# Optimization experiments

Hardware: AMD Instinct MI355X
Metric: run time of the kernel (lower is better)

The kernel has to match this reference:

```python
import jax, jax.numpy as jnp
import numpy as np

B, IN, N, E = 2048, 1024, 64, 128
NEG_SLOPE = 0.01  # torch LeakyReLU default

def setup_inputs() -> dict:
    key = jax.random.key(0)
    k = jax.random.split(key, 5)
    scale_in = 1.0 / np.sqrt(IN)
    scale_ctx = 1.0 / np.sqrt(2 * E)
    return {
        "x": jax.random.normal(k[0], (B, IN), dtype=jnp.float32),
        # stacked per-concept Linear(in_features, 2*emb_size)
        "W_ctx": jax.random.uniform(k[1], (N, IN, 2 * E), jnp.float32, -scale_in, scale_in),
        "b_ctx": jax.random.uniform(k[2], (N, 2 * E), jnp.float32, -scale_in, scale_in),
        # shared Linear(2*emb_size, 1)
        "w_prob": jax.random.uniform(k[3], (2 * E,), jnp.float32, -scale_ctx, scale_ctx),
        "b_prob": jax.random.uniform(k[4], (), jnp.float32, -scale_ctx, scale_ctx),
    }

def reference(x, W_ctx, b_ctx, w_prob, b_prob):
    # context: [B, N, 2E] = LeakyReLU(x @ W_i + b_i) for all concepts i at once
    ctx = jnp.einsum("bi,nio->bno", x, W_ctx) + b_ctx
    ctx = jnp.where(ctx >= 0, ctx, NEG_SLOPE * ctx)
    # shared gate: [B, N]
    c_pred = jax.nn.sigmoid(jnp.einsum("bno,o->bn", ctx, w_prob) + b_prob)
    # gated blend of positive/negative halves -> [B, N, E]
    p = c_pred[..., None]
    c_emb = ctx[..., :E] * p + ctx[..., E:] * (1.0 - p)
    return c_emb, c_pred
```

## Files before the change

### kernel.cpp

```cpp
#include <hip/hip_runtime.h>
#include <hip/hip_bf16.h>

typedef __attribute__((ext_vector_type(4))) short short4v;
typedef __attribute__((ext_vector_type(8))) short short8v;
typedef __attribute__((ext_vector_type(4))) float floatx4;

#define B_ROWS 2048
#define K_DIM  1024
#define N_CON  64
#define TWO_E  256
#define E_DIM  128
#define BM     128
#define BK     64
#define LDSA_BYTES (BM * BK * 2)
#define LDSB_BYTES (TWO_E * BK * 2)
#define SMEM_BYTES (LDSA_BYTES + LDSB_BYTES)
#define EMB_ELEMS 16777216ULL
#define WT_BYTES  33554432ULL
#define XB_BYTES  4194304ULL

static __device__ inline unsigned short bf16bits(float f) {
    __hip_bfloat16 h = __float2bfloat16(f);
    unsigned short u;
    __builtin_memcpy(&u, &h, 2);
    return u;
}

static __device__ inline void dma16(const void* g, void* l) {
    __builtin_amdgcn_global_load_lds(
        (const __attribute__((address_space(1))) unsigned int*)g,
        (__attribute__((address_space(3))) unsigned int*)l,
        16, 0, 0);
}

__global__ void __launch_bounds__(256) prep(const float* __restrict__ W,
                                            const float* __restrict__ x,
                                            unsigned short* __restrict__ Wt,
                                            unsigned short* __restrict__ xb) {
    __shared__ unsigned int lds2[64 * 36];
    const int tid = threadIdx.x;
    const int ot = blockIdx.x, ktile = blockIdx.y, n = blockIdx.z;
    const float* src = W + ((size_t)n * K_DIM + (size_t)ktile * 64) * TWO_E + ot * 64;
    unsigned short* dst = Wt + ((size_t)n * TWO_E + (size_t)ot * 64) * K_DIM + ktile * 64;

    const int kp = tid >> 4;
    const int c  = (tid & 15) * 4;
#pragma unroll
    for (int it = 0; it < 2; ++it) {
        const int k0 = it * 32 + kp * 2;
        floatx4 r0 = *(const floatx4*)&src[(size_t)k0 * TWO_E + c];
        floatx4 r1 = *(const floatx4*)&src[(size_t)(k0 + 1) * TWO_E + c];
#pragma unroll
        for (int j = 0; j < 4; ++j) {
            unsigned int d = (unsigned int)bf16bits(r0[j]) |
                             ((unsigned int)bf16bits(r1[j]) << 16);
            lds2[(c + j) * 36 + it * 16 + kp] = d;
        }
    }
    __syncthreads();
#pragma unroll
    for (int it = 0; it < 2; ++it) {
        int q = it * 256 + tid;
        int o = q >> 3, kc = q & 7;
        short8v v = *(short8v*)&lds2[o * 36 + kc * 4];
        *(short8v*)&dst[(size_t)o * K_DIM + kc * 8] = v;
    }

    const int bid = blockIdx.x + blockIdx.y * 4 + blockIdx.z * 64;
    const size_t base = (size_t)bid * 512 + (size_t)tid * 2;
    unsigned int d = (unsigned int)bf16bits(x[base]) |
                     ((unsigned int)bf16bits(x[base + 1]) << 16);
    ((unsigned int*)xb)[base >> 1] = d;
}

template <bool PRET>
__global__ void __launch_bounds__(512, 4)
concept_kernel(const float* __restrict__ x,
               const unsigned short* __restrict__ xb,
               const float* __restrict__ Wc,
               const unsigned short* __restrict__ Wt,
               const float* __restrict__ bc,
               const float* __restrict__ wp,
               const float* __restrict__ bp,
               float* __restrict__ out) {
    __shared__ __align__(16) char smem[SMEM_BYTES];
    char* ldsA = smem;
    char* ldsB = smem + LDSA_BYTES;

    const int tid  = threadIdx.x;
    const int wave = tid >> 6;
    const int lane = tid & 63;
    const int lg   = lane >> 4;
    const int l15  = lane & 15;
    const int h    = wave >> 2;
    const int og   = wave & 3;
    const int rb = blockIdx.x;
    const int n  = blockIdx.y;

    int otile[4];
#pragma unroll
    for (int oi = 0; oi < 4; ++oi) otile[oi] = og * 32 + (oi & 1) * 16 + (oi & 2) * 64;

    floatx4 acc[4][4];
#pragma unroll
    for (int mi = 0; mi < 4; ++mi)
#pragma unroll
        for (int oi = 0; oi < 4; ++oi) acc[mi][oi] = (floatx4){0.f, 0.f, 0.f, 0.f};

    const unsigned short* xrow  = PRET ? xb + (size_t)rb * BM * K_DIM : nullptr;
    const unsigned short* wbase = PRET ? Wt + (size_t)n * TWO_E * K_DIM : nullptr;
    const float* xg = x + (size_t)rb * BM * K_DIM;
    const float* wg = Wc + (size_t)n * K_DIM * TWO_E;

    for (int kt = 0; kt < K_DIM; kt += BK) {
        if (PRET) {
#pragma unroll
            for (int it = 0; it < 2; ++it) {
                int c = it * 8 + wave;
                int s = c * 64 + lane;
                int r = s >> 3, g = s & 7;
                dma16(xrow + (size_t)r * K_DIM + kt + ((g ^ (r & 7)) * 8),
                      ldsA + c * 1024);
            }
#pragma unroll
            for (int it = 0; it < 4; ++it) {
                int c = it * 8 + wave;
                int s = c * 64 + lane;
                int r = s >> 3, g = s & 7;
                dma16(wbase + (size_t)r * K_DIM + kt + ((g ^ (r & 7)) * 8),
                      ldsB + c * 1024);
            }
        } else {
#pragma unroll
            for (int it = 0; it < 2; ++it) {
                int s = it * 512 + tid;
                int r = s >> 3, g = s & 7;
                const float* p = xg + (size_t)r * K_DIM + kt + ((g ^ (r & 7)) * 8);
                floatx4 v0 = *(const floatx4*)p, v1 = *(const floatx4*)(p + 4);
                short8v b;
                b[0] = (short)bf16bits(v0[0]); b[1] = (short)bf16bits(v0[1]);
                b[2] = (short)bf16bits(v0[2]); b[3] = (short)bf16bits(v0[3]);
                b[4] = (short)bf16bits(v1[0]); b[5] = (short)bf16bits(v1[1]);
                b[6] = (short)bf16bits(v1[2]); b[7] = (short)bf16bits(v1[3]);
                *(short8v*)(ldsA + s * 16) = b;
            }
#pragma unroll
            for (int it = 0; it < 4; ++it) {
                int s = it * 512 + tid;
                int r = s >> 3, g = s & 7;
                int k0 = kt + (g ^ (r & 7)) * 8;
                short8v b;
#pragma unroll
                for (int j = 0; j < 8; ++j)
                    b[j] = (short)bf16bits(wg[(size_t)(k0 + j) * TWO_E + r]);
                *(short8v*)(ldsB + s * 16) = b;
            }
        }
        __syncthreads();

#pragma unroll
        for (int ks = 0; ks < 2; ++ks) {
            const int sw = ((ks * 4 + lg) ^ (l15 & 7)) * 16;
            short8v af[4], bfr[4];
#pragma unroll
            for (int mi = 0; mi < 4; ++mi)
                af[mi] = *(const short8v*)(ldsA + (h * 64 + mi * 16 + l15) * 128 + sw);
#pragma unroll
            for (int oi = 0; oi < 4; ++oi)
                bfr[oi] = *(const short8v*)(ldsB + (otile[oi] + l15) * 128 + sw);
#pragma unroll
            for (int mi = 0; mi < 4; ++mi)
#pragma unroll
                for (int oi = 0; oi < 4; ++oi)
                    acc[mi][oi] = __builtin_amdgcn_mfma_f32_16x16x32_bf16(
                        af[mi], bfr[oi], acc[mi][oi], 0, 0, 0);
        }
        __syncthreads();
    }

    float biasf[4], wpf[4];
#pragma unroll
    for (int oi = 0; oi < 4; ++oi) {
        int o = otile[oi] + l15;
        biasf[oi] = bc[n * TWO_E + o];
        wpf[oi]  = wp[o];
    }
#pragma unroll
    for (int mi = 0; mi < 4; ++mi)
#pragma unroll
        for (int oi = 0; oi < 4; ++oi)
#pragma unroll
            for (int j = 0; j < 4; ++j) {
                float v = acc[mi][oi][j] + biasf[oi];
                acc[mi][oi][j] = v >= 0.f ? v : 0.01f * v;
            }

    float* partial = (float*)smem;
    float* pv      = (float*)(smem + 2048);

#pragma unroll
    for (int mi = 0; mi < 4; ++mi)
#pragma unroll
        for (int j = 0; j < 4; ++j) {
            float ps = 0.f;
#pragma unroll
            for (int oi = 0; oi < 4; ++oi) ps += acc[mi][oi][j] * wpf[oi];
            ps += __shfl_xor(ps, 1);
            ps += __shfl_xor(ps, 2);
            ps += __shfl_xor(ps, 4);
            ps += __shfl_xor(ps, 8);
            if (l15 == 0) partial[(h * 64 + mi * 16 + lg * 4 + j) * 4 + og] = ps;
        }
    __syncthreads();

    if (tid < 128) {
        float s = partial[tid * 4] + partial[tid * 4 + 1] + partial[tid * 4 + 2] +
                  partial[tid * 4 + 3] + bp[0];
        float p = 1.f / (1.f + __expf(-s));
        pv[tid] = p;
        size_t bi = (size_t)rb * BM + tid;
        out[EMB_ELEMS + bi * N_CON + n] = p;
    }
    __syncthreads();

#pragma unroll
    for (int mi = 0; mi < 4; ++mi)
#pragma unroll
        for (int oi = 0; oi < 2; ++oi)
#pragma unroll
            for (int j = 0; j < 4; ++j) {
                int row = h * 64 + mi * 16 + lg * 4 + j;
                int e = og * 32 + oi * 16 + l15;
                float p = pv[row];
                float v = acc[mi][oi][j] * p + acc[mi][oi + 2][j] * (1.f - p);
                size_t bi = (size_t)rb * BM + row;
                out[(bi * N_CON + n) * E_DIM + e] = v;
            }
}

extern "C" void kernel_launch(void* const* d_in, const int* in_sizes, int n_in,
                              void* d_out, int out_size, void* d_ws, size_t ws_size,
                              hipStream_t stream) {
    const float* x  = (const float*)d_in[0];
    const float* Wc = (const float*)d_in[1];
    const float* bc = (const float*)d_in[2];
    const float* wp = (const float*)d_in[3];
    const float* bp = (const float*)d_in[4];
    float* out = (float*)d_out;

    if (ws_size >= WT_BYTES + XB_BYTES) {
        unsigned short* Wt = (unsigned short*)d_ws;
        unsigned short* xb = (unsigned short*)((char*)d_ws + WT_BYTES);
        prep<<<dim3(4, 16, 64), 256, 0, stream>>>(Wc, x, Wt, xb);
        concept_kernel<true><<<dim3(16, 64), 512, 0, stream>>>(
            x, xb, Wc, Wt, bc, wp, bp, out);
    } else {
        concept_kernel<false><<<dim3(16, 64), 512, 0, stream>>>(
            x, nullptr, Wc, nullptr, bc, wp, bp, out);
    }
}
```

Before: 197.6 us.

## Add triple-buffered async-DMA pipelined GEMM kernel with block swizzle

```diff
diff --git a/kernel.cpp b/kernel.cpp
--- a/kernel.cpp
+++ b/kernel.cpp
@@ -12,9 +12,12 @@
 #define E_DIM  128
 #define BM     128
 #define BK     64
+#define NT     16
 #define LDSA_BYTES (BM * BK * 2)
 #define LDSB_BYTES (TWO_E * BK * 2)
-#define SMEM_BYTES (LDSA_BYTES + LDSB_BYTES)
+#define TILE_BYTES (LDSA_BYTES + LDSB_BYTES)
+#define NBUF 3
+#define SMEM_DYN (TILE_BYTES * NBUF)
 #define EMB_ELEMS 16777216ULL
 #define WT_BYTES  33554432ULL
 #define XB_BYTES  4194304ULL
@@ -73,17 +76,210 @@
     ((unsigned int*)xb)[base >> 1] = d;
 }
 
-template <bool PRET>
+static __device__ inline void stage_A(const unsigned short* xrow, int kt,
+                                      char* ldsA, int wave, int lane) {
+#pragma unroll
+    for (int it = 0; it < 2; ++it) {
+        int c = it * 8 + wave;
+        int s = c * 64 + lane;
+        int r = s >> 3, g = s & 7;
+        dma16(xrow + (size_t)r * K_DIM + kt + ((g ^ (r & 7)) * 8), ldsA + c * 1024);
+    }
+}
+
+template <int I0, int I1>
+static __device__ inline void stage_B(const unsigned short* wbase, int kt,
+                                      char* ldsB, int wave, int lane) {
+#pragma unroll
+    for (int it = I0; it < I1; ++it) {
+        int c = it * 8 + wave;
+        int s = c * 64 + lane;
+        int r = s >> 3, g = s & 7;
+        dma16(wbase + (size_t)r * K_DIM + kt + ((g ^ (r & 7)) * 8), ldsB + c * 1024);
+    }
+}
+
+__global__ void __launch_bounds__(512, 2)
+concept_pipe(const unsigned short* __restrict__ xb,
+             const unsigned short* __restrict__ Wt,
+             const float* __restrict__ bc,
+             const float* __restrict__ wp,
+             const float* __restrict__ bp,
+             float* __restrict__ out) {
+    extern __shared__ __align__(16) char smem[];
+
+    const int tid  = threadIdx.x;
+    const int wave = tid >> 6;
+    const int lane = tid & 63;
+    const int lg   = lane >> 4;
+    const int l15  = lane & 15;
+    const int h    = wave >> 2;
+    const int og   = wave & 3;
+
+    const int lin = blockIdx.y * 16 + blockIdx.x;
+    const int nid = (lin & 7) * 128 + (lin >> 3);
+    const int rb  = nid & 15;
+    const int n   = nid >> 4;
+
+    int otile[4];
+#pragma unroll
+    for (int oi = 0; oi < 4; ++oi) otile[oi] = og * 32 + (oi & 1) * 16 + (oi & 2) * 64;
+
+    floatx4 acc[4][4];
+#pragma unroll
+    for (int mi = 0; mi < 4; ++mi)
+#pragma unroll
+        for (int oi = 0; oi < 4; ++oi) acc[mi][oi] = (floatx4){0.f, 0.f, 0.f, 0.f};
+
+    const unsigned short* xrow  = xb + (size_t)rb * BM * K_DIM;
+    const unsigned short* wbase = Wt + (size_t)n * TWO_E * K_DIM;
+
+    stage_A(xrow, 0, smem, wave, lane);
+    stage_B<0, 4>(wbase, 0, smem + LDSA_BYTES, wave, lane);
+    stage_A(xrow, BK, smem + TILE_BYTES, wave, lane);
+    stage_B<0, 4>(wbase, BK, smem + TILE_BYTES + LDSA_BYTES, wave, lane);
+
+    asm volatile("s_waitcnt vmcnt(6)" ::: "memory");
+    __builtin_amdgcn_s_barrier();
+
+    int cur = 0;
+#pragma unroll 1
+    for (int t = 0; t < NT; ++t) {
+        char* ldsA = smem + cur * TILE_BYTES;
+        char* ldsB = ldsA + LDSA_BYTES;
+        int stg = cur + 2; if (stg >= NBUF) stg -= NBUF;
+        char* stgA = smem + stg * TILE_BYTES;
+        char* stgB = stgA + LDSA_BYTES;
+        const int ktn = (t + 2) * BK;
+
+        short8v af[4], bfr[4];
+
+        {
+            const int sw = (lg ^ (l15 & 7)) * 16;
+#pragma unroll
+            for (int mi = 0; mi < 4; ++mi)
+                af[mi] = *(const short8v*)(ldsA + (h * 64 + mi * 16 + l15) * 128 + sw);
+#pragma unroll
+            for (int oi = 0; oi < 4; ++oi)
+                bfr[oi] = *(const short8v*)(ldsB + (otile[oi] + l15) * 128 + sw);
+        }
+        if (t <= NT - 3) {
+            stage_A(xrow, ktn, stgA, wave, lane);
+            stage_B<0, 1>(wbase, ktn, stgB, wave, lane);
+        }
+        __builtin_amdgcn_s_barrier();
+        asm volatile("s_waitcnt lgkmcnt(0)" ::: "memory");
+        __builtin_amdgcn_sched_barrier(0);
+        __builtin_amdgcn_s_setprio(1);
+#pragma unroll
+        for (int mi = 0; mi < 4; ++mi)
+#pragma unroll
+            for (int oi = 0; oi < 4; ++oi)
+                acc[mi][oi] = __builtin_amdgcn_mfma_f32_16x16x32_bf16(
+                    af[mi], bfr[oi], acc[mi][oi], 0, 0, 0);
+        __builtin_amdgcn_s_setprio(0);
+        __builtin_amdgcn_s_barrier();
+
+        {
+            const int sw = ((4 + lg) ^ (l15 & 7)) * 16;
+#pragma unroll
+            for (int mi = 0; mi < 4; ++mi)
+                af[mi] = *(const short8v*)(ldsA + (h * 64 + mi * 16 + l15) * 128 + sw);
+#pragma unroll
+            for (int oi = 0; oi < 4; ++oi)
+                bfr[oi] = *(const short8v*)(ldsB + (otile[oi] + l15) * 128 + sw);
+        }
+        if (t <= NT - 3)
+            stage_B<1, 4>(wbase, ktn, stgB, wave, lane);
+        __builtin_amdgcn_s_barrier();
+        asm volatile("s_waitcnt lgkmcnt(0)" ::: "memory");
+        __builtin_amdgcn_sched_barrier(0);
+        __builtin_amdgcn_s_setprio(1);
+#pragma unroll
+        for (int mi = 0; mi < 4; ++mi)
+#pragma unroll
+            for (int oi = 0; oi < 4; ++oi)
+                acc[mi][oi] = __builtin_amdgcn_mfma_f32_16x16x32_bf16(
+                    af[mi], bfr[oi], acc[mi][oi], 0, 0, 0);
+        __builtin_amdgcn_s_setprio(0);
+
+        if (t <= NT - 3)      asm volatile("s_waitcnt vmcnt(6)" ::: "memory");
+        else if (t == NT - 2) asm volatile("s_waitcnt vmcnt(0)" ::: "memory");
+        if (t < NT - 1) __builtin_amdgcn_s_barrier();
+
+        ++cur; if (cur == NBUF) cur = 0;
+    }
+
+    __syncthreads();
+
+    float biasf[4], wpf[4];
+#pragma unroll
+    for (int oi = 0; oi < 4; ++oi) {
+        int o = otile[oi] + l15;
+        biasf[oi] = bc[n * TWO_E + o];
+        wpf[oi]  = wp[o];
+    }
+#pragma unroll
+    for (int mi = 0; mi < 4; ++mi)
+#pragma unroll
+        for (int oi = 0; oi < 4; ++oi)
+#pragma unroll
+            for (int j = 0; j < 4; ++j) {
+                float v = acc[mi][oi][j] + biasf[oi];
+                acc[mi][oi][j] = v >= 0.f ? v : 0.01f * v;
+            }
+
+    float* partial = (float*)smem;
+    float* pv      = (float*)(smem + 2048);
+
+#pragma unroll
+    for (int mi = 0; mi < 4; ++mi)
+#pragma unroll
+        for (int j = 0; j < 4; ++j) {
+            float ps = 0.f;
+#pragma unroll
+            for (int oi = 0; oi < 4; ++oi) ps += acc[mi][oi][j] * wpf[oi];
+            ps += __shfl_xor(ps, 1);
+            ps += __shfl_xor(ps, 2);
+            ps += __shfl_xor(ps, 4);
+            ps += __shfl_xor(ps, 8);
+            if (l15 == 0) partial[(h * 64 + mi * 16 + lg * 4 + j) * 4 + og] = ps;
+        }
+    __syncthreads();
+
+    if (tid < 128) {
+        float s = partial[tid * 4] + partial[tid * 4 + 1] + partial[tid * 4 + 2] +
+                  partial[tid * 4 + 3] + bp[0];
+        float p = 1.f / (1.f + __expf(-s));
+        pv[tid] = p;
+        size_t bi = (size_t)rb * BM + tid;
+        out[EMB_ELEMS + bi * N_CON + n] = p;
+    }
+    __syncthreads();
+
+#pragma unroll
+    for (int mi = 0; mi < 4; ++mi)
+#pragma unroll
+        for (int oi = 0; oi < 2; ++oi)
+#pragma unroll
+            for (int j = 0; j < 4; ++j) {
+                int row = h * 64 + mi * 16 + lg * 4 + j;
+                int e = og * 32 + oi * 16 + l15;
+                float p = pv[row];
+                float v = acc[mi][oi][j] * p + acc[mi][oi + 2][j] * (1.f - p);
+                size_t bi = (size_t)rb * BM + row;
+                out[(bi * N_CON + n) * E_DIM + e] = v;
+            }
+}
+
 __global__ void __launch_bounds__(512, 4)
-concept_kernel(const float* __restrict__ x,
-               const unsigned short* __restrict__ xb,
-               const float* __restrict__ Wc,
-               const unsigned short* __restrict__ Wt,
-               const float* __restrict__ bc,
-               const float* __restrict__ wp,
-               const float* __restrict__ bp,
-               float* __restrict__ out) {
-    __shared__ __align__(16) char smem[SMEM_BYTES];
+concept_fallback(const float* __restrict__ x,
+                 const float* __restrict__ Wc,
+                 const float* __restrict__ bc,
+                 const float* __restrict__ wp,
+                 const float* __restrict__ bp,
+                 float* __restrict__ out) {
+    __shared__ __align__(16) char smem[TILE_BYTES];
     char* ldsA = smem;
     char* ldsB = smem + LDSA_BYTES;
 
@@ -107,54 +303,33 @@
 #pragma unroll
         for (int oi = 0; oi < 4; ++oi) acc[mi][oi] = (floatx4){0.f, 0.f, 0.f, 0.f};
 
-    const unsigned short* xrow  = PRET ? xb + (size_t)rb * BM * K_DIM : nullptr;
-    const unsigned short* wbase = PRET ? Wt + (size_t)n * TWO_E * K_DIM : nullptr;
     const float* xg = x + (size_t)rb * BM * K_DIM;
     const float* wg = Wc + (size_t)n * K_DIM * TWO_E;
 
     for (int kt = 0; kt < K_DIM; kt += BK) {
-        if (PRET) {
-#pragma unroll
-            for (int it = 0; it < 2; ++it) {
-                int c = it * 8 + wave;
-                int s = c * 64 + lane;
-                int r = s >> 3, g = s & 7;
-                dma16(xrow + (size_t)r * K_DIM + kt + ((g ^ (r & 7)) * 8),
-                      ldsA + c * 1024);
-            }
-#pragma unroll
-            for (int it = 0; it < 4; ++it) {
-                int c = it * 8 + wave;
-                int s = c * 64 + lane;
-                int r = s >> 3, g = s & 7;
-                dma16(wbase + (size_t)r * K_DIM + kt + ((g ^ (r & 7)) * 8),
-                      ldsB + c * 1024);
-            }
-        } else {
-#pragma unroll
-            for (int it = 0; it < 2; ++it) {
-                int s = it * 512 + tid;
-                int r = s >> 3, g = s & 7;
-                const float* p = xg + (size_t)r * K_DIM + kt + ((g ^ (r & 7)) * 8);
-                floatx4 v0 = *(const floatx4*)p, v1 = *(const floatx4*)(p + 4);
-                short8v b;
-                b[0] = (short)bf16bits(v0[0]); b[1] = (short)bf16bits(v0[1]);
-                b[2] = (short)bf16bits(v0[2]); b[3] = (short)bf16bits(v0[3]);
-                b[4] = (short)bf16bits(v1[0]); b[5] = (short)bf16bits(v1[1]);
-                b[6] = (short)bf16bits(v1[2]); b[7] = (short)bf16bits(v1[3]);
-                *(short8v*)(ldsA + s * 16) = b;
-            }
-#pragma unroll
-            for (int it = 0; it < 4; ++it) {
-                int s = it * 512 + tid;
-                int r = s >> 3, g = s & 7;
-                int k0 = kt + (g ^ (r & 7)) * 8;
-                short8v b;
-#pragma unroll
-                for (int j = 0; j < 8; ++j)
-                    b[j] = (short)bf16bits(wg[(size_t)(k0 + j) * TWO_E + r]);
-                *(short8v*)(ldsB + s * 16) = b;
-            }
+#pragma unroll
+        for (int it = 0; it < 2; ++it) {
+            int s = it * 512 + tid;
+            int r = s >> 3, g = s & 7;
+            const float* p = xg + (size_t)r * K_DIM + kt + ((g ^ (r & 7)) * 8);
+            floatx4 v0 = *(const floatx4*)p, v1 = *(const floatx4*)(p + 4);
+            short8v b;
+            b[0] = (short)bf16bits(v0[0]); b[1] = (short)bf16bits(v0[1]);
+            b[2] = (short)bf16bits(v0[2]); b[3] = (short)bf16bits(v0[3]);
+            b[4] = (short)bf16bits(v1[0]); b[5] = (short)bf16bits(v1[1]);
+            b[6] = (short)bf16bits(v1[2]); b[7] = (short)bf16bits(v1[3]);
+            *(short8v*)(ldsA + s * 16) = b;
+        }
+#pragma unroll
+        for (int it = 0; it < 4; ++it) {
+            int s = it * 512 + tid;
+            int r = s >> 3, g = s & 7;
+            int k0 = kt + (g ^ (r & 7)) * 8;
+            short8v b;
+#pragma unroll
+            for (int j = 0; j < 8; ++j)
+                b[j] = (short)bf16bits(wg[(size_t)(k0 + j) * TWO_E + r]);
+            *(short8v*)(ldsB + s * 16) = b;
         }
         __syncthreads();
 
@@ -249,13 +424,20 @@
     float* out = (float*)d_out;
 
     if (ws_size >= WT_BYTES + XB_BYTES) {
+        static bool s_attr_done = false;
+        if (!s_attr_done) {
+            hipFuncSetAttribute((const void*)concept_pipe,
+                                hipFuncAttributeMaxDynamicSharedMemorySize,
+                                SMEM_DYN);
+            s_attr_done = true;
+        }
         unsigned short* Wt = (unsigned short*)d_ws;
         unsigned short* xb = (unsigned short*)((char*)d_ws + WT_BYTES);
         prep<<<dim3(4, 16, 64), 256, 0, stream>>>(Wc, x, Wt, xb);
-        concept_kernel<true><<<dim3(16, 64), 512, 0, stream>>>(
-            x, xb, Wc, Wt, bc, wp, bp, out);
+        concept_pipe<<<dim3(16, 64), 512, SMEM_DYN, stream>>>(
+            xb, Wt, bc, wp, bp, out);
     } else {
-        concept_kernel<false><<<dim3(16, 64), 512, 0, stream>>>(
-            x, nullptr, Wc, nullptr, bc, wp, bp, out);
-    }
-}
+        concept_fallback<<<dim3(16, 64), 512, 0, stream>>>(
+            x, Wc, bc, wp, bp, out);
+    }
+}
```

After: 206.8 us. 1.05x slower.
